# Kernel tuning notes

Measured on AMD Instinct MI355X. Metric: run time of the kernel, lower is better.

Reference implementation:

```python
import jax, jax.numpy as jnp
import numpy as np

BLANK = 0
SIZE_AVERAGE = True


def rnnt_loss(acts, labels, act_lens, label_lens):
    # acts: (B, T, U+1, V) raw logits; warp-transducer applies log_softmax internally
    B, T, U1, V = acts.shape
    U = U1 - 1
    logp = jax.nn.log_softmax(acts, axis=-1)          # (B,T,U1,V)
    lp_blank = logp[..., BLANK]                       # (B,T,U1)
    # emission log-prob of label u at grid point (t,u): logp[b,t,u,labels[b,u]]
    lp_emit = jnp.take_along_axis(
        logp[:, :, :U, :], labels[:, None, :, None].astype(jnp.int32), axis=3
    )[..., 0]                                         # (B,T,U)

    # alpha[0,0]=0 ; alpha[0,u] = sum_{k<u} emit[0,k]
    row0 = jnp.concatenate(
        [jnp.zeros((B, 1), acts.dtype), jnp.cumsum(lp_emit[:, 0, :], axis=1)], axis=1
    )                                                 # (B,U1)

    def outer(prev_row, xs):
        blank_prev, emit_t = xs                       # (B,U1), (B,U)
        fb = prev_row + blank_prev                    # arrive via blank from t-1
        def inner(carry, x):
            fb_u, em_prev = x                         # (B,), (B,)
            a = jnp.logaddexp(fb_u, carry + em_prev)  # blank vs emit path
            return a, a
        _, rest = jax.lax.scan(inner, fb[:, 0], (fb[:, 1:].T, emit_t.T))  # (U,B)
        row = jnp.concatenate([fb[:, :1], rest.T], axis=1)               # (B,U1)
        return row, row

    xs = (jnp.moveaxis(lp_blank[:, :-1, :], 1, 0),   # (T-1,B,U1)
          jnp.moveaxis(lp_emit[:, 1:, :], 1, 0))     # (T-1,B,U)
    _, rows = jax.lax.scan(outer, row0, xs)          # (T-1,B,U1)
    alpha = jnp.concatenate([row0[None], rows], axis=0)  # (T,B,U1)

    b_idx = jnp.arange(B)
    t_idx = act_lens.astype(jnp.int32) - 1
    u_idx = label_lens.astype(jnp.int32)
    loglike = alpha[t_idx, b_idx, u_idx] + lp_blank[b_idx, t_idx, u_idx]
    total = -jnp.sum(loglike)
    if SIZE_AVERAGE:
        total = total / B
    return total.reshape(1)


def setup_inputs() -> dict:
    key = jax.random.key(0)
    k1, k2, k3, k4 = jax.random.split(key, 4)
    B, T, U, V = 8, 256, 100, 128
    acts = jax.random.normal(k1, (B, T, U + 1, V), dtype=jnp.float32)
    labels = jax.random.randint(k2, (B, U), 0, V, dtype=jnp.int64)
    act_lens = jax.random.randint(k3, (B,), T // 2, T + 1, dtype=jnp.int32)
    label_lens = jax.random.randint(k4, (B,), U // 2, U + 1, dtype=jnp.int32)
    return {"acts": acts, "labels": labels, "act_lens": act_lens, "label_lens": label_lens}


def reference(acts, labels, act_lens, label_lens):
    return rnnt_loss(acts, labels, act_lens, label_lens)
```

## Files before the change

kernel.cpp:

```cpp
#include <hip/hip_runtime.h>
#include <math.h>

#define B_DIM  8
#define T_DIM  256
#define U_DIM  100
#define U1_DIM 101
#define V_DIM  128

#define ROWU   128
#define DROWS  432
#define DEPTH  32
#define NEGF   (-8.0e29f)
#define FILLP  0xF122F122u
#define LOG2E  1.4426950408889634f
#define LN2    0.69314718055994530942f

typedef unsigned uv2 __attribute__((ext_vector_type(2)));

__device__ __forceinline__ float logadd2(float a, float b) {
    float m = fmaxf(a, b);
    float e = exp2f(-fabsf(a - b));
    return m + log2f(1.0f + e);
}

__device__ __forceinline__ float lane_shr1(float x) {
    int r = __builtin_amdgcn_update_dpp(0, __builtin_bit_cast(int, x),
                                        0x138 , 0xF, 0xF, true);
    return __builtin_bit_cast(float, r);
}

__device__ __forceinline__ unsigned short f2bf(float f) {
    unsigned u = __builtin_bit_cast(unsigned, f);
    u += 0x7FFF + ((u >> 16) & 1);
    return (unsigned short)(u >> 16);
}

__global__ __launch_bounds__(256) void fill_kernel(uint4* __restrict__ p, int n4,
                                                   int* __restrict__ counter) {
    int i = blockIdx.x * 256 + threadIdx.x;
    if (i < n4) p[i] = make_uint4(FILLP, FILLP, FILLP, FILLP);
    if (i == 0) *counter = 0;
}

__global__ __launch_bounds__(256) void lsm_kernel(
    const float* __restrict__ acts, const int* __restrict__ labels,
    const int* __restrict__ act_lens, const int* __restrict__ label_lens,
    unsigned short* __restrict__ comb, int nrows)
{
    int rid = blockIdx.x * 8 + (threadIdx.x >> 5);
    if (rid >= nrows) return;
    int hl = threadIdx.x & 31;

    int u  = rid % U1_DIM;
    int bt = rid / U1_DIM;
    int b  = bt / T_DIM;
    int t  = bt - b * T_DIM;
    if (t >= act_lens[b] || u > label_lens[b]) return;

    const float* row = acts + (size_t)rid * V_DIM;
    float4 x = *reinterpret_cast<const float4*>(row + 4 * hl);
    float4 y = make_float4(x.x * LOG2E, x.y * LOG2E, x.z * LOG2E, x.w * LOG2E);

    float s = exp2f(y.x) + exp2f(y.y) + exp2f(y.z) + exp2f(y.w);
    #pragma unroll
    for (int off = 16; off; off >>= 1) s += __shfl_xor(s, off);
    float lse2 = log2f(s);

    unsigned short* C = comb + (size_t)b * DROWS * (ROWU * 2);
    int d = t + u + 1;

    if (hl == 0)
        C[(size_t)d * (ROWU * 2) + 2 * u] = f2bf(y.x - lse2);
    if (u < U_DIM) {
        int lab = labels[b * U_DIM + u];
        if (hl == (lab >> 2)) {
            int r = lab & 3;
            float v = (r == 0) ? y.x : (r == 1) ? y.y : (r == 2) ? y.z : y.w;
            C[(size_t)d * (ROWU * 2) + 2 * u + 3] = f2bf(v - lse2);
        }
    }
}

__global__ __launch_bounds__(64, 1) void dp_kernel(
    const unsigned* __restrict__ comb,
    const int* __restrict__ act_lens, const int* __restrict__ label_lens,
    float* __restrict__ loglike, int* __restrict__ counter,
    float* __restrict__ out)
{
    const int b = blockIdx.x;
    const int l = threadIdx.x;
    const int tl   = act_lens[b] - 1;
    const int ul   = label_lens[b];
    const int dfin = tl + ul;
    const unsigned* Cb = comb + (size_t)b * DROWS * ROWU + 2 * l;

    unsigned fbu = comb[(size_t)b * DROWS * ROWU + (size_t)(dfin + 1) * ROWU + ul];
    float fin_bl = __builtin_bit_cast(float, fbu << 16);

    float v0 = (l == 0) ? 0.0f : NEGF;
    float v1 = NEGF;
    float rf0 = NEGF, rf1 = NEGF;

    asm volatile("s_waitcnt vmcnt(0)" ::: "memory");

    uv2 r[DEPTH];
    #pragma unroll
    for (int j = 0; j < DEPTH; ++j) {
        const unsigned* p = Cb + (size_t)(1 + j) * ROWU;
        asm volatile("global_load_dwordx2 %0, %1, off" : "=v"(r[j]) : "v"(p));
    }

    const int ngroups = (dfin + DEPTH - 1) / DEPTH;
    int d0 = 1;
    for (int g = 0; g < ngroups; ++g, d0 += DEPTH) {
        #pragma unroll
        for (int J = 0; J < DEPTH; ++J) {
            asm volatile("s_waitcnt vmcnt(31)");
            __builtin_amdgcn_sched_barrier(0);
            uv2 c = r[J];
            float bl0 = __builtin_bit_cast(float, c.x << 16);
            float em0 = __builtin_bit_cast(float, c.x & 0xFFFF0000u);
            float bl1 = __builtin_bit_cast(float, c.y << 16);
            float em1 = __builtin_bit_cast(float, c.y & 0xFFFF0000u);
            float left0 = lane_shr1(v1);
            float a0 = v0 + bl0, p0 = left0 + em0;
            float a1 = v1 + bl1, p1 = v0 + em1;
            v0 = logadd2(a0, p0);
            v1 = logadd2(a1, p1);
            if (d0 + J == dfin) { rf0 = v0; rf1 = v1; }
            const unsigned* p = Cb + (size_t)(d0 + J + DEPTH) * ROWU;
            asm volatile("global_load_dwordx2 %0, %1, off" : "=v"(r[J]) : "v"(p));
        }
    }

    float res = (ul & 1) ? rf1 : rf0;
    if (l == (ul >> 1)) {
        loglike[b] = LN2 * (res + fin_bl);
        __threadfence();
        int old = atomicAdd(counter, 1);
        if (old == B_DIM - 1) {
            __threadfence();
            float s = 0.0f;
            #pragma unroll
            for (int i = 0; i < B_DIM; ++i)
                s += __hip_atomic_load(&loglike[i], __ATOMIC_RELAXED,
                                       __HIP_MEMORY_SCOPE_AGENT);
            out[0] = -s / (float)B_DIM;
        }
    }
}

extern "C" void kernel_launch(void* const* d_in, const int* in_sizes, int n_in,
                              void* d_out, int out_size, void* d_ws, size_t ws_size,
                              hipStream_t stream) {
    const float* acts       = (const float*)d_in[0];
    const int*   labels     = (const int*)d_in[1];
    const int*   act_lens   = (const int*)d_in[2];
    const int*   label_lens = (const int*)d_in[3];

    unsigned* comb    = (unsigned*)d_ws;
    float*    loglike = (float*)(comb + (size_t)B_DIM * DROWS * ROWU);
    int*      counter = (int*)(loglike + B_DIM);

    int nrows   = B_DIM * T_DIM * U1_DIM;
    int nblocks = (nrows + 7) / 8;

    int nfill4  = (B_DIM * DROWS * ROWU) / 4;
    fill_kernel<<<(nfill4 + 255) / 256, 256, 0, stream>>>((uint4*)comb, nfill4, counter);
    lsm_kernel<<<nblocks, 256, 0, stream>>>(acts, labels, act_lens, label_lens,
                                            (unsigned short*)comb, nrows);
    dp_kernel<<<B_DIM, 64, 0, stream>>>(comb, act_lens, label_lens,
                                        loglike, counter, (float*)d_out);
}
```

Baseline: 59.77 us.

## Precompute two-step diagonal transition weights so DP advances two diagonals per iteration

```diff
diff --git a/kernel.cpp b/kernel.cpp
--- a/kernel.cpp
+++ b/kernel.cpp
@@ -9,13 +9,19 @@
 
 #define ROWU   128
 #define DROWS  432
-#define DEPTH  32
+#define WROWC  128
+#define WROWS  428
+#define NW_USED 355
+#define DEPTH  16
 #define NEGF   (-8.0e29f)
 #define FILLP  0xF122F122u
 #define LOG2E  1.4426950408889634f
 #define LN2    0.69314718055994530942f
 
 typedef unsigned uv2 __attribute__((ext_vector_type(2)));
+typedef unsigned uv4 __attribute__((ext_vector_type(4)));
+
+__device__ __forceinline__ float ubit(unsigned u) { return __builtin_bit_cast(float, u); }
 
 __device__ __forceinline__ float logadd2(float a, float b) {
     float m = fmaxf(a, b);
@@ -23,16 +29,22 @@
     return m + log2f(1.0f + e);
 }
 
+__device__ __forceinline__ float lse3(float a, float b, float c) {
+    float m = fmaxf(fmaxf(a, b), c);
+    float s = exp2f(a - m) + exp2f(b - m) + exp2f(c - m);
+    return m + log2f(s);
+}
+
 __device__ __forceinline__ float lane_shr1(float x) {
     int r = __builtin_amdgcn_update_dpp(0, __builtin_bit_cast(int, x),
                                         0x138 , 0xF, 0xF, true);
     return __builtin_bit_cast(float, r);
 }
 
-__device__ __forceinline__ unsigned short f2bf(float f) {
+__device__ __forceinline__ unsigned f2bf(float f) {
     unsigned u = __builtin_bit_cast(unsigned, f);
     u += 0x7FFF + ((u >> 16) & 1);
-    return (unsigned short)(u >> 16);
+    return u >> 16;
 }
 
 __global__ __launch_bounds__(256) void fill_kernel(uint4* __restrict__ p, int n4,
@@ -70,66 +82,119 @@
     int d = t + u + 1;
 
     if (hl == 0)
-        C[(size_t)d * (ROWU * 2) + 2 * u] = f2bf(y.x - lse2);
+        C[(size_t)d * (ROWU * 2) + 2 * u] = (unsigned short)f2bf(y.x - lse2);
     if (u < U_DIM) {
         int lab = labels[b * U_DIM + u];
         if (hl == (lab >> 2)) {
             int r = lab & 3;
             float v = (r == 0) ? y.x : (r == 1) ? y.y : (r == 2) ? y.z : y.w;
-            C[(size_t)d * (ROWU * 2) + 2 * u + 3] = f2bf(v - lse2);
+            C[(size_t)d * (ROWU * 2) + 2 * u + 3] = (unsigned short)f2bf(v - lse2);
         }
     }
 }
 
+__global__ __launch_bounds__(256) void w_kernel(
+    const unsigned* __restrict__ comb, unsigned* __restrict__ W)
+{
+    int wid = blockIdx.x * 4 + (threadIdx.x >> 6);
+    int l   = threadIdx.x & 63;
+    int b   = wid / NW_USED;
+    int ri  = wid - b * NW_USED;
+    int dt  = ri + 2;
+
+    const unsigned* C  = comb + ((size_t)b * DROWS + dt) * ROWU;
+    const unsigned* Cm = C - ROWU;
+
+    uv2 c0 = *(const uv2*)(C  + 2 * l);
+    uv2 cm = *(const uv2*)(Cm + 2 * l);
+    float BL0a = ubit(c0.x << 16), EM0a = ubit(c0.x & 0xFFFF0000u);
+    float BL0b = ubit(c0.y << 16), EM0b = ubit(c0.y & 0xFFFF0000u);
+    float BLma = ubit(cm.x << 16), EMma = ubit(cm.x & 0xFFFF0000u);
+    float BLmb = ubit(cm.y << 16), EMmb = ubit(cm.y & 0xFFFF0000u);
+    float BLmp = lane_shr1(BLmb);
+    float EMmp = lane_shr1(EMmb);
+
+    float wtA = BLma + BL0a;
+    float wmA = logadd2(EMma + BL0a, BLmp + EM0a);
+    float wlA = EMmp + EM0a;
+    float wtB = BLmb + BL0b;
+    float wmB = logadd2(EMmb + BL0b, BLma + EM0b);
+    float wlB = EMma + EM0b;
+
+    if (l == 0) { wmA = NEGF; wlA = NEGF; wlB = NEGF; }
+    if (l >= 52) { wtA = wmA = wlA = wtB = wmB = wlB = NEGF; }
+
+    uv4 o;
+    o.x = f2bf(wtA) | (f2bf(wmA) << 16);
+    o.y = f2bf(wlA);
+    o.z = f2bf(wtB) | (f2bf(wmB) << 16);
+    o.w = f2bf(wlB);
+    *(uv4*)(W + ((size_t)b * WROWS + ri) * (WROWC * 2) + 4 * l) = o;
+}
+
 __global__ __launch_bounds__(64, 1) void dp_kernel(
-    const unsigned* __restrict__ comb,
+    const unsigned* __restrict__ comb, const unsigned* __restrict__ W,
     const int* __restrict__ act_lens, const int* __restrict__ label_lens,
     float* __restrict__ loglike, int* __restrict__ counter,
     float* __restrict__ out)
 {
     const int b = blockIdx.x;
     const int l = threadIdx.x;
-    const int tl   = act_lens[b] - 1;
-    const int ul   = label_lens[b];
-    const int dfin = tl + ul;
-    const unsigned* Cb = comb + (size_t)b * DROWS * ROWU + 2 * l;
-
-    unsigned fbu = comb[(size_t)b * DROWS * ROWU + (size_t)(dfin + 1) * ROWU + ul];
-    float fin_bl = __builtin_bit_cast(float, fbu << 16);
-
-    float v0 = (l == 0) ? 0.0f : NEGF;
-    float v1 = NEGF;
+    const int tl    = act_lens[b] - 1;
+    const int ul    = label_lens[b];
+    const int dfin  = tl + ul;
+    const int start = dfin & 1;
+    const int niter = dfin >> 1;
+
+    const unsigned* combB = comb + (size_t)b * DROWS * ROWU;
+    const char* Wbl = (const char*)(W + (size_t)b * WROWS * (WROWC * 2)) + 16 * l;
+
+    unsigned fbu = combB[(size_t)(dfin + 1) * ROWU + ul];
+    float fin_bl = ubit(fbu << 16);
+    unsigned i0 = combB[ROWU + 0];
+    unsigned i1 = combB[ROWU + 1];
+
+    float v0 = NEGF, v1 = NEGF;
+    if (l == 0) {
+        v0 = start ? ubit(i0 << 16) : 0.0f;
+        v1 = start ? ubit(i1 & 0xFFFF0000u) : NEGF;
+    }
     float rf0 = NEGF, rf1 = NEGF;
 
     asm volatile("s_waitcnt vmcnt(0)" ::: "memory");
 
-    uv2 r[DEPTH];
+    uv4 rW[DEPTH];
     #pragma unroll
     for (int j = 0; j < DEPTH; ++j) {
-        const unsigned* p = Cb + (size_t)(1 + j) * ROWU;
-        asm volatile("global_load_dwordx2 %0, %1, off" : "=v"(r[j]) : "v"(p));
-    }
-
-    const int ngroups = (dfin + DEPTH - 1) / DEPTH;
-    int d0 = 1;
-    for (int g = 0; g < ngroups; ++g, d0 += DEPTH) {
+        const char* p = Wbl + (size_t)(start + 2 * j) * 1024;
+        asm volatile("global_load_dwordx4 %0, %1, off" : "=v"(rW[j]) : "v"(p));
+    }
+
+    const int ngroups = (niter + DEPTH - 1) / DEPTH;
+    for (int g = 0; g < ngroups; ++g) {
+        const int it0 = g * DEPTH;
+        const char* gb = Wbl + (size_t)(start + 2 * it0 + 2 * DEPTH) * 1024;
         #pragma unroll
-        for (int J = 0; J < DEPTH; ++J) {
-            asm volatile("s_waitcnt vmcnt(31)");
+        for (int q = 0; q < 4; ++q) {
+            asm volatile("s_waitcnt vmcnt(12)");
             __builtin_amdgcn_sched_barrier(0);
-            uv2 c = r[J];
-            float bl0 = __builtin_bit_cast(float, c.x << 16);
-            float em0 = __builtin_bit_cast(float, c.x & 0xFFFF0000u);
-            float bl1 = __builtin_bit_cast(float, c.y << 16);
-            float em1 = __builtin_bit_cast(float, c.y & 0xFFFF0000u);
-            float left0 = lane_shr1(v1);
-            float a0 = v0 + bl0, p0 = left0 + em0;
-            float a1 = v1 + bl1, p1 = v0 + em1;
-            v0 = logadd2(a0, p0);
-            v1 = logadd2(a1, p1);
-            if (d0 + J == dfin) { rf0 = v0; rf1 = v1; }
-            const unsigned* p = Cb + (size_t)(d0 + J + DEPTH) * ROWU;
-            asm volatile("global_load_dwordx2 %0, %1, off" : "=v"(r[J]) : "v"(p));
+            #pragma unroll
+            for (int j4 = 0; j4 < 4; ++j4) {
+                const int J = q * 4 + j4;
+                uv4 w = rW[J];
+                float wtA = ubit(w.x << 16), wmA = ubit(w.x & 0xFFFF0000u);
+                float wlA = ubit(w.y << 16);
+                float wtB = ubit(w.z << 16), wmB = ubit(w.z & 0xFFFF0000u);
+                float wlB = ubit(w.w << 16);
+                float s1 = lane_shr1(v1);
+                float s0 = lane_shr1(v0);
+                float nA = lse3(v0 + wtA, s1 + wmA, s0 + wlA);
+                float nB = lse3(v1 + wtB, v0 + wmB, s1 + wlB);
+                if (it0 + J == niter - 1) { rf0 = nA; rf1 = nB; }
+                v0 = nA; v1 = nB;
+                const char* p = gb + (size_t)(2 * J) * 1024;
+                asm volatile("global_load_dwordx4 %0, %1, off" : "=v"(rW[J]) : "v"(p));
+            }
         }
     }
 
@@ -159,7 +224,8 @@
     const int*   label_lens = (const int*)d_in[3];
 
     unsigned* comb    = (unsigned*)d_ws;
-    float*    loglike = (float*)(comb + (size_t)B_DIM * DROWS * ROWU);
+    unsigned* W       = comb + (size_t)B_DIM * DROWS * ROWU;
+    float*    loglike = (float*)(W + (size_t)B_DIM * WROWS * (WROWC * 2));
     int*      counter = (int*)(loglike + B_DIM);
 
     int nrows   = B_DIM * T_DIM * U1_DIM;
@@ -169,6 +235,8 @@
     fill_kernel<<<(nfill4 + 255) / 256, 256, 0, stream>>>((uint4*)comb, nfill4, counter);
     lsm_kernel<<<nblocks, 256, 0, stream>>>(acts, labels, act_lens, label_lens,
                                             (unsigned short*)comb, nrows);
-    dp_kernel<<<B_DIM, 64, 0, stream>>>(comb, act_lens, label_lens,
+    int wwaves  = B_DIM * NW_USED;
+    w_kernel<<<(wwaves + 3) / 4, 256, 0, stream>>>(comb, W);
+    dp_kernel<<<B_DIM, 64, 0, stream>>>(comb, W, act_lens, label_lens,
                                         loglike, counter, (float*)d_out);
 }
```

Result: faster. 58.51 us (-2.1%).

## Precompose four anti-diagonal DP steps into transfer weights to shorten serial chain

Applied to the files above, without the earlier changes.

```diff
diff --git a/kernel.cpp b/kernel.cpp
--- a/kernel.cpp
+++ b/kernel.cpp
@@ -8,8 +8,12 @@
 #define V_DIM  128
 
 #define ROWU   128
-#define DROWS  432
-#define DEPTH  32
+#define DROWS  360
+#define NV     352
+#define VROWS  418
+#define VROWB  1280
+#define PL     416
+#define DEPTH  16
 #define NEGF   (-8.0e29f)
 #define FILLP  0xF122F122u
 #define LOG2E  1.4426950408889634f
@@ -17,11 +21,23 @@
 
 typedef unsigned uv2 __attribute__((ext_vector_type(2)));
 
+__device__ __forceinline__ float ubit(unsigned u) { return __builtin_bit_cast(float, u); }
+
 __device__ __forceinline__ float logadd2(float a, float b) {
     float m = fmaxf(a, b);
     float e = exp2f(-fabsf(a - b));
     return m + log2f(1.0f + e);
 }
+__device__ __forceinline__ float lse3(float a, float b, float c) {
+    float m = fmaxf(fmaxf(a, b), c);
+    float s = exp2f(a - m) + exp2f(b - m) + exp2f(c - m);
+    return m + log2f(s);
+}
+__device__ __forceinline__ float lse5(float a, float b, float c, float d, float e) {
+    float m = fmaxf(fmaxf(fmaxf(a, b), c), fmaxf(d, e));
+    float s = exp2f(a - m) + exp2f(b - m) + exp2f(c - m) + exp2f(d - m) + exp2f(e - m);
+    return m + log2f(s);
+}
 
 __device__ __forceinline__ float lane_shr1(float x) {
     int r = __builtin_amdgcn_update_dpp(0, __builtin_bit_cast(int, x),
@@ -29,10 +45,28 @@
     return __builtin_bit_cast(float, r);
 }
 
-__device__ __forceinline__ unsigned short f2bf(float f) {
+__device__ __forceinline__ unsigned f2bf(float f) {
     unsigned u = __builtin_bit_cast(unsigned, f);
     u += 0x7FFF + ((u >> 16) & 1);
-    return (unsigned short)(u >> 16);
+    return u >> 16;
+}
+
+struct W2 { float tA, mA, lA, tB, mB, lB; };
+__device__ __forceinline__ W2 buildW2(uv2 c0 , uv2 cm , int l) {
+    float BL0a = ubit(c0.x << 16), EM0a = ubit(c0.x & 0xFFFF0000u);
+    float BL0b = ubit(c0.y << 16), EM0b = ubit(c0.y & 0xFFFF0000u);
+    float BLma = ubit(cm.x << 16), EMma = ubit(cm.x & 0xFFFF0000u);
+    float BLmb = ubit(cm.y << 16), EMmb = ubit(cm.y & 0xFFFF0000u);
+    float BLmp = lane_shr1(BLmb), EMmp = lane_shr1(EMmb);
+    W2 w;
+    w.tA = BLma + BL0a;
+    w.mA = logadd2(EMma + BL0a, BLmp + EM0a);
+    w.lA = EMmp + EM0a;
+    w.tB = BLmb + BL0b;
+    w.mB = logadd2(EMmb + BL0b, BLma + EM0b);
+    w.lB = EMma + EM0b;
+    if (l == 0) { w.mA = NEGF; w.lA = NEGF; w.lB = NEGF; }
+    return w;
 }
 
 __global__ __launch_bounds__(256) void fill_kernel(uint4* __restrict__ p, int n4,
@@ -70,66 +104,141 @@
     int d = t + u + 1;
 
     if (hl == 0)
-        C[(size_t)d * (ROWU * 2) + 2 * u] = f2bf(y.x - lse2);
+        C[(size_t)d * (ROWU * 2) + 2 * u] = (unsigned short)f2bf(y.x - lse2);
     if (u < U_DIM) {
         int lab = labels[b * U_DIM + u];
         if (hl == (lab >> 2)) {
             int r = lab & 3;
             float v = (r == 0) ? y.x : (r == 1) ? y.y : (r == 2) ? y.z : y.w;
-            C[(size_t)d * (ROWU * 2) + 2 * u + 3] = f2bf(v - lse2);
+            C[(size_t)d * (ROWU * 2) + 2 * u + 3] = (unsigned short)f2bf(v - lse2);
         }
     }
 }
 
+__global__ __launch_bounds__(256) void v_kernel(
+    const unsigned* __restrict__ comb, unsigned* __restrict__ V)
+{
+    int wid = blockIdx.x * 4 + (threadIdx.x >> 6);
+    if (wid >= B_DIM * NV) return;
+    int l  = threadIdx.x & 63;
+    int b  = wid / NV;
+    int ri = wid - b * NV;
+    int dt = ri + 4;
+
+    const unsigned* C = comb + ((size_t)b * DROWS + dt) * ROWU + 2 * l;
+    uv2 c0 = *(const uv2*)(C);
+    uv2 c1 = *(const uv2*)(C - ROWU);
+    uv2 c2 = *(const uv2*)(C - 2 * ROWU);
+    uv2 c3 = *(const uv2*)(C - 3 * ROWU);
+
+    W2 P = buildW2(c0, c1, l);
+    W2 Q = buildW2(c2, c3, l);
+
+    float Qt_b1 = lane_shr1(Q.tB), Qm_b1 = lane_shr1(Q.mB), Ql_b1 = lane_shr1(Q.lB);
+    float Qt_a1 = lane_shr1(Q.tA), Qm_a1 = lane_shr1(Q.mA), Ql_a1 = lane_shr1(Q.lA);
+
+    float V0a = P.tA + Q.tA;
+    float V1a = logadd2(P.tA + Q.mA, P.mA + Qt_b1);
+    float V2a = lse3(P.tA + Q.lA, P.mA + Qm_b1, P.lA + Qt_a1);
+    float V3a = logadd2(P.mA + Ql_b1, P.lA + Qm_a1);
+    float V4a = P.lA + Ql_a1;
+    float V0b = P.tB + Q.tB;
+    float V1b = logadd2(P.tB + Q.mB, P.mB + Q.tA);
+    float V2b = lse3(P.tB + Q.lB, P.mB + Q.mA, P.lB + Qt_b1);
+    float V3b = logadd2(P.mB + Q.lA, P.lB + Qm_b1);
+    float V4b = P.lB + Ql_b1;
+
+    if (l == 0) { V1a = NEGF; V2a = NEGF; V3a = NEGF; V4a = NEGF; }
+
+    if (l < 52) {
+        char* row = (char*)V + ((size_t)b * VROWS + ri) * VROWB + 8 * l;
+        uv2 p0, p1, p2;
+        p0.x = f2bf(V0a) | (f2bf(V1a) << 16);  p0.y = f2bf(V0b) | (f2bf(V1b) << 16);
+        p1.x = f2bf(V2a) | (f2bf(V3a) << 16);  p1.y = f2bf(V2b) | (f2bf(V3b) << 16);
+        p2.x = f2bf(V4a);                      p2.y = f2bf(V4b);
+        *(uv2*)(row)          = p0;
+        *(uv2*)(row + PL)     = p1;
+        *(uv2*)(row + 2 * PL) = p2;
+    }
+}
+
 __global__ __launch_bounds__(64, 1) void dp_kernel(
-    const unsigned* __restrict__ comb,
+    const unsigned* __restrict__ comb, const unsigned* __restrict__ V,
     const int* __restrict__ act_lens, const int* __restrict__ label_lens,
     float* __restrict__ loglike, int* __restrict__ counter,
     float* __restrict__ out)
 {
     const int b = blockIdx.x;
     const int l = threadIdx.x;
-    const int tl   = act_lens[b] - 1;
-    const int ul   = label_lens[b];
-    const int dfin = tl + ul;
-    const unsigned* Cb = comb + (size_t)b * DROWS * ROWU + 2 * l;
-
-    unsigned fbu = comb[(size_t)b * DROWS * ROWU + (size_t)(dfin + 1) * ROWU + ul];
-    float fin_bl = __builtin_bit_cast(float, fbu << 16);
+    const int tl    = act_lens[b] - 1;
+    const int ul    = label_lens[b];
+    const int dfin  = tl + ul;
+    const int start = dfin & 3;
+    const int niter = dfin >> 2;
+
+    const unsigned* combB = comb + (size_t)b * DROWS * ROWU;
+    const char* Vb = (const char*)V + (size_t)b * VROWS * VROWB + 8 * l;
+
+    unsigned fbu = combB[(size_t)(dfin + 1) * ROWU + ul];
+    float fin_bl = ubit(fbu << 16);
 
     float v0 = (l == 0) ? 0.0f : NEGF;
     float v1 = NEGF;
+    for (int d = 1; d <= start; ++d) {
+        uv2 c = *(const uv2*)(combB + (size_t)d * ROWU + 2 * l);
+        float bl0 = ubit(c.x << 16), em0 = ubit(c.x & 0xFFFF0000u);
+        float bl1 = ubit(c.y << 16), em1 = ubit(c.y & 0xFFFF0000u);
+        float left0 = lane_shr1(v1);
+        float a0 = v0 + bl0, p0 = left0 + em0;
+        float a1 = v1 + bl1, p1 = v0 + em1;
+        v0 = logadd2(a0, p0);
+        v1 = logadd2(a1, p1);
+    }
     float rf0 = NEGF, rf1 = NEGF;
 
     asm volatile("s_waitcnt vmcnt(0)" ::: "memory");
 
-    uv2 r[DEPTH];
+    uv2 r0[DEPTH], r1[DEPTH], r2[DEPTH];
     #pragma unroll
     for (int j = 0; j < DEPTH; ++j) {
-        const unsigned* p = Cb + (size_t)(1 + j) * ROWU;
-        asm volatile("global_load_dwordx2 %0, %1, off" : "=v"(r[j]) : "v"(p));
-    }
-
-    const int ngroups = (dfin + DEPTH - 1) / DEPTH;
-    int d0 = 1;
-    for (int g = 0; g < ngroups; ++g, d0 += DEPTH) {
+        int rr = start + 4 * j; rr = rr < VROWS - 2 ? rr : VROWS - 3;
+        const char* p = Vb + (size_t)rr * VROWB;
+        asm volatile("global_load_dwordx2 %0, %1, off" : "=v"(r0[j]) : "v"(p));
+        asm volatile("global_load_dwordx2 %0, %1, off" : "=v"(r1[j]) : "v"(p + PL));
+        asm volatile("global_load_dwordx2 %0, %1, off" : "=v"(r2[j]) : "v"(p + 2 * PL));
+    }
+
+    const int ngroups = (niter + DEPTH - 1) / DEPTH;
+    for (int g = 0; g < ngroups; ++g) {
+        const int it0 = g * DEPTH;
         #pragma unroll
-        for (int J = 0; J < DEPTH; ++J) {
-            asm volatile("s_waitcnt vmcnt(31)");
+        for (int q = 0; q < 4; ++q) {
+            asm volatile("s_waitcnt vmcnt(36)");
             __builtin_amdgcn_sched_barrier(0);
-            uv2 c = r[J];
-            float bl0 = __builtin_bit_cast(float, c.x << 16);
-            float em0 = __builtin_bit_cast(float, c.x & 0xFFFF0000u);
-            float bl1 = __builtin_bit_cast(float, c.y << 16);
-            float em1 = __builtin_bit_cast(float, c.y & 0xFFFF0000u);
-            float left0 = lane_shr1(v1);
-            float a0 = v0 + bl0, p0 = left0 + em0;
-            float a1 = v1 + bl1, p1 = v0 + em1;
-            v0 = logadd2(a0, p0);
-            v1 = logadd2(a1, p1);
-            if (d0 + J == dfin) { rf0 = v0; rf1 = v1; }
-            const unsigned* p = Cb + (size_t)(d0 + J + DEPTH) * ROWU;
-            asm volatile("global_load_dwordx2 %0, %1, off" : "=v"(r[J]) : "v"(p));
+            #pragma unroll
+            for (int j4 = 0; j4 < 4; ++j4) {
+                const int J = q * 4 + j4;
+                const int it = it0 + J;
+                uv2 a0 = r0[J], a1 = r1[J], a2 = r2[J];
+                float V0a = ubit(a0.x << 16), V1a = ubit(a0.x & 0xFFFF0000u);
+                float V0b = ubit(a0.y << 16), V1b = ubit(a0.y & 0xFFFF0000u);
+                float V2a = ubit(a1.x << 16), V3a = ubit(a1.x & 0xFFFF0000u);
+                float V2b = ubit(a1.y << 16), V3b = ubit(a1.y & 0xFFFF0000u);
+                float V4a = ubit(a2.x << 16), V4b = ubit(a2.y << 16);
+                float s1 = lane_shr1(v1);
+                float s0 = lane_shr1(v0);
+                float s3 = lane_shr1(s1);
+                float s2 = lane_shr1(s0);
+                float nA = lse5(v0 + V0a, s1 + V1a, s0 + V2a, s3 + V3a, s2 + V4a);
+                float nB = lse5(v1 + V0b, v0 + V1b, s1 + V2b, s0 + V3b, s3 + V4b);
+                if (it == niter - 1) { rf0 = nA; rf1 = nB; }
+                v0 = nA; v1 = nB;
+                int rr = start + 4 * (it + DEPTH); rr = rr < VROWS - 2 ? rr : VROWS - 3;
+                const char* p = Vb + (size_t)rr * VROWB;
+                asm volatile("global_load_dwordx2 %0, %1, off" : "=v"(r0[J]) : "v"(p));
+                asm volatile("global_load_dwordx2 %0, %1, off" : "=v"(r1[J]) : "v"(p + PL));
+                asm volatile("global_load_dwordx2 %0, %1, off" : "=v"(r2[J]) : "v"(p + 2 * PL));
+            }
         }
     }
 
@@ -159,7 +268,8 @@
     const int*   label_lens = (const int*)d_in[3];
 
     unsigned* comb    = (unsigned*)d_ws;
-    float*    loglike = (float*)(comb + (size_t)B_DIM * DROWS * ROWU);
+    unsigned* V       = comb + (size_t)B_DIM * DROWS * ROWU;
+    float*    loglike = (float*)((char*)V + (size_t)B_DIM * VROWS * VROWB);
     int*      counter = (int*)(loglike + B_DIM);
 
     int nrows   = B_DIM * T_DIM * U1_DIM;
@@ -169,6 +279,8 @@
     fill_kernel<<<(nfill4 + 255) / 256, 256, 0, stream>>>((uint4*)comb, nfill4, counter);
     lsm_kernel<<<nblocks, 256, 0, stream>>>(acts, labels, act_lens, label_lens,
                                             (unsigned short*)comb, nrows);
-    dp_kernel<<<B_DIM, 64, 0, stream>>>(comb, act_lens, label_lens,
+    int vwaves = B_DIM * NV;
+    v_kernel<<<(vwaves + 3) / 4, 256, 0, stream>>>(comb, V);
+    dp_kernel<<<B_DIM, 64, 0, stream>>>(comb, V, act_lens, label_lens,
                                         loglike, counter, (float*)d_out);
 }
```

Result: faster. 56.91 us (-4.8%).
